# Kernel tuning notes

Measured on AMD Instinct MI355X. Metric: run time of the kernel, lower is better.

Reference implementation:

```python
import jax, jax.numpy as jnp
import numpy as np

B, N, K, C, CE, H = 2, 2048, 48, 128, 128, 128
IN = 2 * C + CE  # 384
AGG_SCALE = 30.0
LN_EPS = 1e-5


def setup_inputs() -> dict:
    key = jax.random.key(0)
    ks = jax.random.split(key, 12)
    inp = {
        "node_h": jax.random.normal(ks[0], (B, N, C), jnp.float32),
        "edge_h": jax.random.normal(ks[1], (B, N, K, CE), jnp.float32),
        "edge_index": jax.random.randint(ks[2], (B, N, K), 0, N, jnp.int64),
        # message MLP: Linear(IN,H) GELU Linear(H,H) GELU Linear(H,C)
        "W1": jax.random.normal(ks[3], (IN, H), jnp.float32) / np.sqrt(IN),
        "b1": jnp.zeros((H,), jnp.float32),
        "W2": jax.random.normal(ks[4], (H, H), jnp.float32) / np.sqrt(H),
        "b2": jnp.zeros((H,), jnp.float32),
        "W3": jax.random.normal(ks[5], (H, C), jnp.float32) / np.sqrt(H),
        "b3": jnp.zeros((C,), jnp.float32),
        "Wu": jax.random.normal(ks[6], (C, C), jnp.float32) / np.sqrt(C),
        "bu": jnp.zeros((C,), jnp.float32),
        "ln_g": jnp.ones((C,), jnp.float32),
        "ln_b": jnp.zeros((C,), jnp.float32),
    }
    return inp


def _layer_norm(x, g, b):
    mu = jnp.mean(x, axis=-1, keepdims=True)
    var = jnp.var(x, axis=-1, keepdims=True)
    return (x - mu) * jax.lax.rsqrt(var + LN_EPS) * g + b


def _gelu(x):
    return jax.nn.gelu(x, approximate=False)  # torch nn.GELU default (erf)


def reference(node_h, edge_h, edge_index, W1, b1, W2, b2, W3, b3, Wu, bu, ln_g, ln_b):
    b, n, k = edge_index.shape
    c = node_h.shape[-1]
    # gather neighbor node features: (B,N,K,C)
    node_j = jnp.take_along_axis(
        node_h, edge_index.reshape(b, n * k)[..., None], axis=1
    ).reshape(b, n, k, c)
    node_i = jnp.broadcast_to(node_h[:, :, None, :], (b, n, k, c))
    edge_packed = jnp.concatenate([node_i, node_j, edge_h], axis=-1)  # (B,N,K,IN)
    # message MLP
    h = _gelu(edge_packed @ W1 + b1)
    h = _gelu(h @ W2 + b2)
    messages = (h @ W3 + b3).sum(axis=-2) / AGG_SCALE  # (B,N,C)
    # dropout is identity in eval mode
    updated_nodes = _layer_norm(node_h + messages, ln_g, ln_b)
    node_updates = updated_nodes @ Wu + bu
    out = _layer_norm(node_h + node_updates, ln_g, ln_b)
    return out
```

## Files before the change

### kernel.cpp

```cpp
#include <hip/hip_runtime.h>
#include <hip/hip_bf16.h>
#include <math.h>

#define Bn   2
#define Nn   2048
#define Kn   48
#define Cn   128

typedef short bf16x8 __attribute__((ext_vector_type(8)));
typedef float f32x4  __attribute__((ext_vector_type(4)));

#if __has_builtin(__builtin_amdgcn_cvt_pk_bf16_f32)
#define HAS_PK 1
#endif

__device__ __forceinline__ short f2bf(float f) {
  union { float f; unsigned u; } v; v.f = f;
  unsigned r = v.u + 0x7fffu + ((v.u >> 16) & 1u);
  return (short)(r >> 16);
}

__device__ __forceinline__ unsigned pk2(float a, float b) {
#ifdef HAS_PK
  auto p = __builtin_amdgcn_cvt_pk_bf16_f32(a, b);
  return __builtin_bit_cast(unsigned, p);
#else
  return (unsigned)(unsigned short)f2bf(a) | ((unsigned)(unsigned short)f2bf(b) << 16);
#endif
}

__device__ __forceinline__ float gelu_f(float x) {
  float z = x * (-2.3021991f - 0.10294200f * x * x);
  float e = __builtin_amdgcn_exp2f(z);
  return x * __builtin_amdgcn_rcpf(1.0f + e);
}

__global__ void pack_weights(const float* __restrict__ W1,
                             const float* __restrict__ W2,
                             const float* __restrict__ W3,
                             const float* __restrict__ Wu,
                             short* __restrict__ ws) {
  int tid = blockIdx.x * blockDim.x + threadIdx.x;
  if (tid >= 192 * 64) return;
  int lane = tid & 63;
  int tile = tid >> 6;
  const float* W; short* dst;
  if (tile < 32)       { W = W1;               dst = ws; }
  else if (tile < 96)  { W = W1 + 16384;       dst = ws + 16384; tile -= 32; }
  else if (tile < 128) { W = W2;               dst = ws + 49152; tile -= 96; }
  else if (tile < 160) { W = W3;               dst = ws + 65536; tile -= 128; }
  else                 { W = Wu;               dst = ws + 81920; tile -= 160; }
  int kt = tile >> 3, nt = tile & 7;
  int n  = nt * 16 + (lane & 15);
  int k0 = kt * 32 + (lane >> 4) * 8;
  union { short s[8]; bf16x8 v; } u8;
#pragma unroll
  for (int j = 0; j < 8; j++) u8.s[j] = f2bf(W[(k0 + j) * 128 + n]);
  *reinterpret_cast<bf16x8*>(dst + (tile << 9) + lane * 8) = u8.v;
}

__device__ __forceinline__ void block_reduce2(float v1, float v2, float* red,
                                              int tid, float& o1, float& o2) {
#pragma unroll
  for (int off = 32; off >= 1; off >>= 1) {
    v1 += __shfl_xor(v1, off);
    v2 += __shfl_xor(v2, off);
  }
  if ((tid & 63) == 0) { red[tid >> 6] = v1; red[4 + (tid >> 6)] = v2; }
  __syncthreads();
  o1 = red[0] + red[1] + red[2] + red[3];
  o2 = red[4] + red[5] + red[6] + red[7];
  __syncthreads();
}

__global__ __launch_bounds__(256, 6)
void node_update_kernel(const float* __restrict__ node_h,
                        const float* __restrict__ edge_h,
                        const int*   __restrict__ edge_index,
                        const short* __restrict__ wpack,
                        const float* __restrict__ b1,
                        const float* __restrict__ b2,
                        const float* __restrict__ b3,
                        const float* __restrict__ bu,
                        const float* __restrict__ ln_g,
                        const float* __restrict__ ln_b,
                        float* __restrict__ out) {
  __shared__ __align__(16) char smem[26592];
  short* Xs    = (short*)smem;
  short* H1s   = (short*)(smem + 12288);
  short* nhb   = (short*)(smem + 24576);
  float* nhs   = (float*)(smem + 24832);
  int*   idx_s = (int*)  (smem + 25344);
  float* msg_s = (float*)(smem + 25536);
  short* hsb   = (short*)(smem + 26048);
  short* ub    = (short*)(smem + 26304);
  float* red_s = (float*)(smem + 26560);

  const int tid  = threadIdx.x;
  const int blk  = blockIdx.x;
  const int bb   = blk >> 11;
  const int lane = tid & 63;
  const int wave = tid >> 6;
  const int lr   = lane & 15;
  const int lq   = lane >> 4;

  const short* W1i = wpack;
  const short* W1e = wpack + 16384;
  const short* W2p = wpack + 49152;
  const short* W3p = wpack + 65536;
  const short* Wup = wpack + 81920;

  if (tid < 128) {
    float v = node_h[(size_t)blk * Cn + tid];
    nhs[tid] = v;
    nhb[tid] = f2bf(v);
  } else if (tid < 176) {
    idx_s[tid - 128] = edge_index[blk * Kn + (tid - 128)];
  }
  __syncthreads();

#pragma unroll
  for (int i = tid; i < 48 * 32; i += 256) {
    int r = i >> 5;
    int w = i & 31;
    const float* src = (w < 16)
        ? node_h + (size_t)(bb * Nn + idx_s[r]) * Cn + w * 8
        : edge_h + ((size_t)blk * Kn + r) * Cn + (w - 16) * 8;
    float4 v0 = *reinterpret_cast<const float4*>(src);
    float4 v1 = *reinterpret_cast<const float4*>(src + 4);
    uint4 p;
    p.x = pk2(v0.x, v0.y); p.y = pk2(v0.z, v0.w);
    p.z = pk2(v1.x, v1.y); p.w = pk2(v1.z, v1.w);
    *reinterpret_cast<uint4*>(&Xs[r * 256 + ((w ^ (r & 7)) << 3)]) = p;
  }

  f32x4 accY[2] = {};
#pragma unroll
  for (int kt = 0; kt < 4; kt++) {
    bf16x8 av = {};
    if (lr == 0) av = *reinterpret_cast<const bf16x8*>(&nhb[kt * 32 + lq * 8]);
    bf16x8 bv0 = *reinterpret_cast<const bf16x8*>(W1i + ((kt * 8 + wave * 2 + 0) << 9) + lane * 8);
    bf16x8 bv1 = *reinterpret_cast<const bf16x8*>(W1i + ((kt * 8 + wave * 2 + 1) << 9) + lane * 8);
    accY[0] = __builtin_amdgcn_mfma_f32_16x16x32_bf16(av, bv0, accY[0], 0, 0, 0);
    accY[1] = __builtin_amdgcn_mfma_f32_16x16x32_bf16(av, bv1, accY[1], 0, 0, 0);
  }
  __syncthreads();

  f32x4 acc[3][2] = {};
#pragma unroll
  for (int kt = 0; kt < 8; kt++) {
    bf16x8 bf0 = *reinterpret_cast<const bf16x8*>(W1e + ((kt * 8 + wave * 2 + 0) << 9) + lane * 8);
    bf16x8 bf1 = *reinterpret_cast<const bf16x8*>(W1e + ((kt * 8 + wave * 2 + 1) << 9) + lane * 8);
    int sw = (((kt * 4 + lq) ^ (lr & 7)) << 3);
    bf16x8 a0 = *reinterpret_cast<const bf16x8*>(&Xs[(0  + lr) * 256 + sw]);
    bf16x8 a1 = *reinterpret_cast<const bf16x8*>(&Xs[(16 + lr) * 256 + sw]);
    bf16x8 a2 = *reinterpret_cast<const bf16x8*>(&Xs[(32 + lr) * 256 + sw]);
    acc[0][0] = __builtin_amdgcn_mfma_f32_16x16x32_bf16(a0, bf0, acc[0][0], 0, 0, 0);
    acc[0][1] = __builtin_amdgcn_mfma_f32_16x16x32_bf16(a0, bf1, acc[0][1], 0, 0, 0);
    acc[1][0] = __builtin_amdgcn_mfma_f32_16x16x32_bf16(a1, bf0, acc[1][0], 0, 0, 0);
    acc[1][1] = __builtin_amdgcn_mfma_f32_16x16x32_bf16(a1, bf1, acc[1][1], 0, 0, 0);
    acc[2][0] = __builtin_amdgcn_mfma_f32_16x16x32_bf16(a2, bf0, acc[2][0], 0, 0, 0);
    acc[2][1] = __builtin_amdgcn_mfma_f32_16x16x32_bf16(a2, bf1, acc[2][1], 0, 0, 0);
  }
  __syncthreads();

#pragma unroll
  for (int j = 0; j < 2; j++) {
    int col = (wave * 2 + j) * 16 + lr;
    float yi = __shfl(accY[j][0], lr) + b1[col];
    int g = col >> 3, cl = col & 7;
#pragma unroll
    for (int mt = 0; mt < 3; mt++) {
      int r0 = mt * 16 + lq * 4;
      float g0 = gelu_f(acc[mt][j][0] + yi);
      float g1 = gelu_f(acc[mt][j][1] + yi);
      float g2 = gelu_f(acc[mt][j][2] + yi);
      float g3 = gelu_f(acc[mt][j][3] + yi);
      unsigned p01 = pk2(g0, g1), p23 = pk2(g2, g3);
      H1s[(r0 + 0) * 128 + ((g ^ ((r0 + 0) & 7)) << 3) + cl] = (short)(p01 & 0xffff);
      H1s[(r0 + 1) * 128 + ((g ^ ((r0 + 1) & 7)) << 3) + cl] = (short)(p01 >> 16);
      H1s[(r0 + 2) * 128 + ((g ^ ((r0 + 2) & 7)) << 3) + cl] = (short)(p23 & 0xffff);
      H1s[(r0 + 3) * 128 + ((g ^ ((r0 + 3) & 7)) << 3) + cl] = (short)(p23 >> 16);
    }
  }
  __syncthreads();

  f32x4 acc2[3][2] = {};
#pragma unroll
  for (int kt = 0; kt < 4; kt++) {
    bf16x8 bf0 = *reinterpret_cast<const bf16x8*>(W2p + ((kt * 8 + wave * 2 + 0) << 9) + lane * 8);
    bf16x8 bf1 = *reinterpret_cast<const bf16x8*>(W2p + ((kt * 8 + wave * 2 + 1) << 9) + lane * 8);
    int sw = (((kt * 4 + lq) ^ (lr & 7)) << 3);
    bf16x8 a0 = *reinterpret_cast<const bf16x8*>(&H1s[(0  + lr) * 128 + sw]);
    bf16x8 a1 = *reinterpret_cast<const bf16x8*>(&H1s[(16 + lr) * 128 + sw]);
    bf16x8 a2 = *reinterpret_cast<const bf16x8*>(&H1s[(32 + lr) * 128 + sw]);
    acc2[0][0] = __builtin_amdgcn_mfma_f32_16x16x32_bf16(a0, bf0, acc2[0][0], 0, 0, 0);
    acc2[0][1] = __builtin_amdgcn_mfma_f32_16x16x32_bf16(a0, bf1, acc2[0][1], 0, 0, 0);
    acc2[1][0] = __builtin_amdgcn_mfma_f32_16x16x32_bf16(a1, bf0, acc2[1][0], 0, 0, 0);
    acc2[1][1] = __builtin_amdgcn_mfma_f32_16x16x32_bf16(a1, bf1, acc2[1][1], 0, 0, 0);
    acc2[2][0] = __builtin_amdgcn_mfma_f32_16x16x32_bf16(a2, bf0, acc2[2][0], 0, 0, 0);
    acc2[2][1] = __builtin_amdgcn_mfma_f32_16x16x32_bf16(a2, bf1, acc2[2][1], 0, 0, 0);
  }
#pragma unroll
  for (int j = 0; j < 2; j++) {
    int col = (wave * 2 + j) * 16 + lr;
    float bias = b2[col];
    float s = 0.f;
#pragma unroll
    for (int mt = 0; mt < 3; mt++)
#pragma unroll
      for (int r = 0; r < 4; r++) s += gelu_f(acc2[mt][j][r] + bias);
    s += __shfl_xor(s, 16);
    s += __shfl_xor(s, 32);
    if (lq == 0) hsb[col] = f2bf(s);
  }
  __syncthreads();

  f32x4 accM[2] = {};
#pragma unroll
  for (int kt = 0; kt < 4; kt++) {
    bf16x8 av = {};
    if (lr == 0) av = *reinterpret_cast<const bf16x8*>(&hsb[kt * 32 + lq * 8]);
    bf16x8 bv0 = *reinterpret_cast<const bf16x8*>(W3p + ((kt * 8 + wave * 2 + 0) << 9) + lane * 8);
    bf16x8 bv1 = *reinterpret_cast<const bf16x8*>(W3p + ((kt * 8 + wave * 2 + 1) << 9) + lane * 8);
    accM[0] = __builtin_amdgcn_mfma_f32_16x16x32_bf16(av, bv0, accM[0], 0, 0, 0);
    accM[1] = __builtin_amdgcn_mfma_f32_16x16x32_bf16(av, bv1, accM[1], 0, 0, 0);
  }
  if (lq == 0) {
#pragma unroll
    for (int j = 0; j < 2; j++) {
      int col = (wave * 2 + j) * 16 + lr;
      msg_s[col] = (accM[j][0] + 48.0f * b3[col]) * (1.0f / 30.0f);
    }
  }
  __syncthreads();

  const int c    = tid & 127;
  const int half = tid >> 7;
  float nh = nhs[c];
  float x  = (half == 0) ? (nh + msg_s[c]) : 0.f;
  float sum, sumsq;
  block_reduce2(x, x * x, red_s, tid, sum, sumsq);
  float mu   = sum * (1.f / 128.f);
  float var  = sumsq * (1.f / 128.f) - mu * mu;
  float rstd = rsqrtf(var + 1e-5f);
  if (half == 0) ub[c] = f2bf((x - mu) * rstd * ln_g[c] + ln_b[c]);
  __syncthreads();

  f32x4 accU[2] = {};
#pragma unroll
  for (int kt = 0; kt < 4; kt++) {
    bf16x8 av = {};
    if (lr == 0) av = *reinterpret_cast<const bf16x8*>(&ub[kt * 32 + lq * 8]);
    bf16x8 bv0 = *reinterpret_cast<const bf16x8*>(Wup + ((kt * 8 + wave * 2 + 0) << 9) + lane * 8);
    bf16x8 bv1 = *reinterpret_cast<const bf16x8*>(Wup + ((kt * 8 + wave * 2 + 1) << 9) + lane * 8);
    accU[0] = __builtin_amdgcn_mfma_f32_16x16x32_bf16(av, bv0, accU[0], 0, 0, 0);
    accU[1] = __builtin_amdgcn_mfma_f32_16x16x32_bf16(av, bv1, accU[1], 0, 0, 0);
  }
  if (lq == 0) {
#pragma unroll
    for (int j = 0; j < 2; j++) {
      int col = (wave * 2 + j) * 16 + lr;
      msg_s[col] = accU[j][0] + bu[col];
    }
  }
  __syncthreads();

  float y = (half == 0) ? (nh + msg_s[c]) : 0.f;
  float sum2, sumsq2;
  block_reduce2(y, y * y, red_s, tid, sum2, sumsq2);
  float mu2   = sum2 * (1.f / 128.f);
  float var2  = sumsq2 * (1.f / 128.f) - mu2 * mu2;
  float rstd2 = rsqrtf(var2 + 1e-5f);
  if (half == 0)
    out[(size_t)blk * Cn + c] = (y - mu2) * rstd2 * ln_g[c] + ln_b[c];
}

extern "C" void kernel_launch(void* const* d_in, const int* in_sizes, int n_in,
                              void* d_out, int out_size, void* d_ws, size_t ws_size,
                              hipStream_t stream) {
  const float* node_h     = (const float*)d_in[0];
  const float* edge_h     = (const float*)d_in[1];
  const int*   edge_index = (const int*)  d_in[2];
  const float* W1 = (const float*)d_in[3];
  const float* b1 = (const float*)d_in[4];
  const float* W2 = (const float*)d_in[5];
  const float* b2 = (const float*)d_in[6];
  const float* W3 = (const float*)d_in[7];
  const float* b3 = (const float*)d_in[8];
  const float* Wu = (const float*)d_in[9];
  const float* bu = (const float*)d_in[10];
  const float* ln_g = (const float*)d_in[11];
  const float* ln_b = (const float*)d_in[12];
  float* out   = (float*)d_out;
  short* wpack = (short*)d_ws;

  pack_weights<<<48, 256, 0, stream>>>(W1, W2, W3, Wu, wpack);
  node_update_kernel<<<Bn * Nn, 256, 0, stream>>>(
      node_h, edge_h, edge_index, wpack,
      b1, b2, b3, bu, ln_g, ln_b, out);
}
```

Baseline: 215.4 us.

## Split per-node tail into batched 16-row kernel with full MFMA tiles

The per-node MLP kernel now stops after the second GELU layer and its K-sum, and writes the fp32 hidden sums into the output buffer. A new tail kernel processes 16 nodes per block. It runs W3, LayerNorm, Wu and the second LayerNorm using full 16-row MFMA tiles and per-wave shuffle reductions, instead of single-row MFMAs with block-wide reductions. This removes several barriers and wasted MFMA rows from the main kernel and cuts its LDS use. The cost is an extra launch and a global round trip of the intermediate through the output buffer.

```diff
diff --git a/kernel.cpp b/kernel.cpp
--- a/kernel.cpp
+++ b/kernel.cpp
@@ -6,6 +6,7 @@
 #define Nn   2048
 #define Kn   48
 #define Cn   128
+#define G2   16
 
 typedef short bf16x8 __attribute__((ext_vector_type(8)));
 typedef float f32x4  __attribute__((ext_vector_type(4)));
@@ -45,11 +46,11 @@
   int lane = tid & 63;
   int tile = tid >> 6;
   const float* W; short* dst;
-  if (tile < 32)       { W = W1;               dst = ws; }
-  else if (tile < 96)  { W = W1 + 16384;       dst = ws + 16384; tile -= 32; }
-  else if (tile < 128) { W = W2;               dst = ws + 49152; tile -= 96; }
-  else if (tile < 160) { W = W3;               dst = ws + 65536; tile -= 128; }
-  else                 { W = Wu;               dst = ws + 81920; tile -= 160; }
+  if (tile < 32)       { W = W1;         dst = ws; }
+  else if (tile < 96)  { W = W1 + 16384; dst = ws + 16384; tile -= 32; }
+  else if (tile < 128) { W = W2;         dst = ws + 49152; tile -= 96; }
+  else if (tile < 160) { W = W3;         dst = ws + 65536; tile -= 128; }
+  else                 { W = Wu;         dst = ws + 81920; tile -= 160; }
   int kt = tile >> 3, nt = tile & 7;
   int n  = nt * 16 + (lane & 15);
   int k0 = kt * 32 + (lane >> 4) * 8;
@@ -57,20 +58,6 @@
 #pragma unroll
   for (int j = 0; j < 8; j++) u8.s[j] = f2bf(W[(k0 + j) * 128 + n]);
   *reinterpret_cast<bf16x8*>(dst + (tile << 9) + lane * 8) = u8.v;
-}
-
-__device__ __forceinline__ void block_reduce2(float v1, float v2, float* red,
-                                              int tid, float& o1, float& o2) {
-#pragma unroll
-  for (int off = 32; off >= 1; off >>= 1) {
-    v1 += __shfl_xor(v1, off);
-    v2 += __shfl_xor(v2, off);
-  }
-  if ((tid & 63) == 0) { red[tid >> 6] = v1; red[4 + (tid >> 6)] = v2; }
-  __syncthreads();
-  o1 = red[0] + red[1] + red[2] + red[3];
-  o2 = red[4] + red[5] + red[6] + red[7];
-  __syncthreads();
 }
 
 __global__ __launch_bounds__(256, 6)
@@ -80,21 +67,12 @@
                         const short* __restrict__ wpack,
                         const float* __restrict__ b1,
                         const float* __restrict__ b2,
-                        const float* __restrict__ b3,
-                        const float* __restrict__ bu,
-                        const float* __restrict__ ln_g,
-                        const float* __restrict__ ln_b,
-                        float* __restrict__ out) {
-  __shared__ __align__(16) char smem[26592];
+                        float* __restrict__ hs_out) {
+  __shared__ __align__(16) char smem[25024];
   short* Xs    = (short*)smem;
   short* H1s   = (short*)(smem + 12288);
   short* nhb   = (short*)(smem + 24576);
-  float* nhs   = (float*)(smem + 24832);
-  int*   idx_s = (int*)  (smem + 25344);
-  float* msg_s = (float*)(smem + 25536);
-  short* hsb   = (short*)(smem + 26048);
-  short* ub    = (short*)(smem + 26304);
-  float* red_s = (float*)(smem + 26560);
+  int*   idx_s = (int*)  (smem + 24832);
 
   const int tid  = threadIdx.x;
   const int blk  = blockIdx.x;
@@ -107,31 +85,30 @@
   const short* W1i = wpack;
   const short* W1e = wpack + 16384;
   const short* W2p = wpack + 49152;
-  const short* W3p = wpack + 65536;
-  const short* Wup = wpack + 81920;
 
   if (tid < 128) {
-    float v = node_h[(size_t)blk * Cn + tid];
-    nhs[tid] = v;
-    nhb[tid] = f2bf(v);
+    nhb[tid] = f2bf(node_h[(size_t)blk * Cn + tid]);
   } else if (tid < 176) {
     idx_s[tid - 128] = edge_index[blk * Kn + (tid - 128)];
   }
   __syncthreads();
 
-#pragma unroll
-  for (int i = tid; i < 48 * 32; i += 256) {
-    int r = i >> 5;
-    int w = i & 31;
-    const float* src = (w < 16)
-        ? node_h + (size_t)(bb * Nn + idx_s[r]) * Cn + w * 8
-        : edge_h + ((size_t)blk * Kn + r) * Cn + (w - 16) * 8;
-    float4 v0 = *reinterpret_cast<const float4*>(src);
-    float4 v1 = *reinterpret_cast<const float4*>(src + 4);
-    uint4 p;
-    p.x = pk2(v0.x, v0.y); p.y = pk2(v0.z, v0.w);
-    p.z = pk2(v1.x, v1.y); p.w = pk2(v1.z, v1.w);
-    *reinterpret_cast<uint4*>(&Xs[r * 256 + ((w ^ (r & 7)) << 3)]) = p;
+  {
+    const int w  = tid & 31;
+    const int rr = tid >> 5;
+#pragma unroll
+    for (int k = 0; k < 6; k++) {
+      int r = rr + k * 8;
+      const float* src = (w < 16)
+          ? node_h + (size_t)(bb * Nn + idx_s[r]) * Cn + w * 8
+          : edge_h + ((size_t)blk * Kn + r) * Cn + (w - 16) * 8;
+      float4 v0 = *reinterpret_cast<const float4*>(src);
+      float4 v1 = *reinterpret_cast<const float4*>(src + 4);
+      uint4 p;
+      p.x = pk2(v0.x, v0.y); p.y = pk2(v0.z, v0.w);
+      p.z = pk2(v1.x, v1.y); p.w = pk2(v1.z, v1.w);
+      *reinterpret_cast<uint4*>(&Xs[r * 256 + ((w ^ (r & 7)) << 3)]) = p;
+    }
   }
 
   f32x4 accY[2] = {};
@@ -212,68 +189,135 @@
       for (int r = 0; r < 4; r++) s += gelu_f(acc2[mt][j][r] + bias);
     s += __shfl_xor(s, 16);
     s += __shfl_xor(s, 32);
-    if (lq == 0) hsb[col] = f2bf(s);
-  }
-  __syncthreads();
-
-  f32x4 accM[2] = {};
+    if (lq == 0) hs_out[(size_t)blk * Cn + col] = s;
+  }
+}
+
+__global__ __launch_bounds__(256, 4)
+void tail_kernel(const float* __restrict__ node_h,
+                 const short* __restrict__ wpack,
+                 const float* __restrict__ b3,
+                 const float* __restrict__ bu,
+                 const float* __restrict__ ln_g,
+                 const float* __restrict__ ln_b,
+                 float* __restrict__ out) {
+  __shared__ __align__(16) char sm2[24832];
+  short* hsB = (short*)sm2;
+  float* nhr = (float*)(sm2 + 4096);
+  float* xs  = (float*)(sm2 + 12288);
+  short* usB = (short*)(sm2 + 20736);
+
+  const int tid  = threadIdx.x;
+  const int lane = tid & 63;
+  const int wave = tid >> 6;
+  const int lr   = lane & 15;
+  const int lq   = lane >> 4;
+  const int n0   = blockIdx.x * G2;
+
+  const short* W3p = wpack + 65536;
+  const short* Wup = wpack + 81920;
+
+  {
+    int row = tid >> 4, seg = tid & 15;
+    const float* p = node_h + (size_t)(n0 + row) * Cn + seg * 8;
+    float4 a0 = *reinterpret_cast<const float4*>(p);
+    float4 a1 = *reinterpret_cast<const float4*>(p + 4);
+    *reinterpret_cast<float4*>(&nhr[row * 128 + seg * 8])     = a0;
+    *reinterpret_cast<float4*>(&nhr[row * 128 + seg * 8 + 4]) = a1;
+    const float* q = out + (size_t)(n0 + row) * Cn + seg * 8;
+    float4 c0 = *reinterpret_cast<const float4*>(q);
+    float4 c1 = *reinterpret_cast<const float4*>(q + 4);
+    uint4 pk;
+    pk.x = pk2(c0.x, c0.y); pk.y = pk2(c0.z, c0.w);
+    pk.z = pk2(c1.x, c1.y); pk.w = pk2(c1.z, c1.w);
+    *reinterpret_cast<uint4*>(&hsB[row * 128 + ((seg ^ (row & 7)) << 3)]) = pk;
+  }
+  __syncthreads();
+
+  f32x4 am[2] = {};
 #pragma unroll
   for (int kt = 0; kt < 4; kt++) {
-    bf16x8 av = {};
-    if (lr == 0) av = *reinterpret_cast<const bf16x8*>(&hsb[kt * 32 + lq * 8]);
+    bf16x8 av = *reinterpret_cast<const bf16x8*>(&hsB[lr * 128 + (((kt * 4 + lq) ^ (lr & 7)) << 3)]);
     bf16x8 bv0 = *reinterpret_cast<const bf16x8*>(W3p + ((kt * 8 + wave * 2 + 0) << 9) + lane * 8);
     bf16x8 bv1 = *reinterpret_cast<const bf16x8*>(W3p + ((kt * 8 + wave * 2 + 1) << 9) + lane * 8);
-    accM[0] = __builtin_amdgcn_mfma_f32_16x16x32_bf16(av, bv0, accM[0], 0, 0, 0);
-    accM[1] = __builtin_amdgcn_mfma_f32_16x16x32_bf16(av, bv1, accM[1], 0, 0, 0);
-  }
-  if (lq == 0) {
-#pragma unroll
-    for (int j = 0; j < 2; j++) {
-      int col = (wave * 2 + j) * 16 + lr;
-      msg_s[col] = (accM[j][0] + 48.0f * b3[col]) * (1.0f / 30.0f);
-    }
-  }
-  __syncthreads();
-
-  const int c    = tid & 127;
-  const int half = tid >> 7;
-  float nh = nhs[c];
-  float x  = (half == 0) ? (nh + msg_s[c]) : 0.f;
-  float sum, sumsq;
-  block_reduce2(x, x * x, red_s, tid, sum, sumsq);
-  float mu   = sum * (1.f / 128.f);
-  float var  = sumsq * (1.f / 128.f) - mu * mu;
-  float rstd = rsqrtf(var + 1e-5f);
-  if (half == 0) ub[c] = f2bf((x - mu) * rstd * ln_g[c] + ln_b[c]);
-  __syncthreads();
-
-  f32x4 accU[2] = {};
+    am[0] = __builtin_amdgcn_mfma_f32_16x16x32_bf16(av, bv0, am[0], 0, 0, 0);
+    am[1] = __builtin_amdgcn_mfma_f32_16x16x32_bf16(av, bv1, am[1], 0, 0, 0);
+  }
+#pragma unroll
+  for (int j = 0; j < 2; j++) {
+    int col = (wave * 2 + j) * 16 + lr;
+    float bb = 48.0f * b3[col];
+#pragma unroll
+    for (int r = 0; r < 4; r++) {
+      int row = lq * 4 + r;
+      xs[row * 132 + col] = nhr[row * 128 + col] + (am[j][r] + bb) * (1.0f / 30.0f);
+    }
+  }
+  __syncthreads();
+
+  const float lg1 = ln_g[lane],      lb1v = ln_b[lane];
+  const float lg2 = ln_g[lane + 64], lb2v = ln_b[lane + 64];
+#pragma unroll
+  for (int s = 0; s < 4; s++) {
+    int row = wave * 4 + s;
+    float v1 = xs[row * 132 + lane];
+    float v2 = xs[row * 132 + lane + 64];
+    float s1 = v1 + v2, s2 = v1 * v1 + v2 * v2;
+#pragma unroll
+    for (int off = 32; off >= 1; off >>= 1) {
+      s1 += __shfl_xor(s1, off);
+      s2 += __shfl_xor(s2, off);
+    }
+    float mu = s1 * (1.f / 128.f);
+    float var = s2 * (1.f / 128.f) - mu * mu;
+    float rstd = rsqrtf(var + 1e-5f);
+    unsigned u12 = pk2((v1 - mu) * rstd * lg1 + lb1v,
+                       (v2 - mu) * rstd * lg2 + lb2v);
+    int sw = (row & 7);
+    usB[row * 128 + (((lane >> 3) ^ sw) << 3) + (lane & 7)]       = (short)(u12 & 0xffff);
+    usB[row * 128 + ((((lane >> 3) + 8) ^ sw) << 3) + (lane & 7)] = (short)(u12 >> 16);
+  }
+  __syncthreads();
+
+  f32x4 au[2] = {};
 #pragma unroll
   for (int kt = 0; kt < 4; kt++) {
-    bf16x8 av = {};
-    if (lr == 0) av = *reinterpret_cast<const bf16x8*>(&ub[kt * 32 + lq * 8]);
+    bf16x8 av = *reinterpret_cast<const bf16x8*>(&usB[lr * 128 + (((kt * 4 + lq) ^ (lr & 7)) << 3)]);
     bf16x8 bv0 = *reinterpret_cast<const bf16x8*>(Wup + ((kt * 8 + wave * 2 + 0) << 9) + lane * 8);
     bf16x8 bv1 = *reinterpret_cast<const bf16x8*>(Wup + ((kt * 8 + wave * 2 + 1) << 9) + lane * 8);
-    accU[0] = __builtin_amdgcn_mfma_f32_16x16x32_bf16(av, bv0, accU[0], 0, 0, 0);
-    accU[1] = __builtin_amdgcn_mfma_f32_16x16x32_bf16(av, bv1, accU[1], 0, 0, 0);
-  }
-  if (lq == 0) {
-#pragma unroll
-    for (int j = 0; j < 2; j++) {
-      int col = (wave * 2 + j) * 16 + lr;
-      msg_s[col] = accU[j][0] + bu[col];
-    }
-  }
-  __syncthreads();
-
-  float y = (half == 0) ? (nh + msg_s[c]) : 0.f;
-  float sum2, sumsq2;
-  block_reduce2(y, y * y, red_s, tid, sum2, sumsq2);
-  float mu2   = sum2 * (1.f / 128.f);
-  float var2  = sumsq2 * (1.f / 128.f) - mu2 * mu2;
-  float rstd2 = rsqrtf(var2 + 1e-5f);
-  if (half == 0)
-    out[(size_t)blk * Cn + c] = (y - mu2) * rstd2 * ln_g[c] + ln_b[c];
+    au[0] = __builtin_amdgcn_mfma_f32_16x16x32_bf16(av, bv0, au[0], 0, 0, 0);
+    au[1] = __builtin_amdgcn_mfma_f32_16x16x32_bf16(av, bv1, au[1], 0, 0, 0);
+  }
+  __syncthreads();
+#pragma unroll
+  for (int j = 0; j < 2; j++) {
+    int col = (wave * 2 + j) * 16 + lr;
+    float bb = bu[col];
+#pragma unroll
+    for (int r = 0; r < 4; r++) {
+      int row = lq * 4 + r;
+      xs[row * 132 + col] = nhr[row * 128 + col] + au[j][r] + bb;
+    }
+  }
+  __syncthreads();
+
+#pragma unroll
+  for (int s = 0; s < 4; s++) {
+    int row = wave * 4 + s;
+    float v1 = xs[row * 132 + lane];
+    float v2 = xs[row * 132 + lane + 64];
+    float s1 = v1 + v2, s2 = v1 * v1 + v2 * v2;
+#pragma unroll
+    for (int off = 32; off >= 1; off >>= 1) {
+      s1 += __shfl_xor(s1, off);
+      s2 += __shfl_xor(s2, off);
+    }
+    float mu = s1 * (1.f / 128.f);
+    float var = s2 * (1.f / 128.f) - mu * mu;
+    float rstd = rsqrtf(var + 1e-5f);
+    out[(size_t)(n0 + row) * Cn + lane]      = (v1 - mu) * rstd * lg1 + lb1v;
+    out[(size_t)(n0 + row) * Cn + lane + 64] = (v2 - mu) * rstd * lg2 + lb2v;
+  }
 }
 
 extern "C" void kernel_launch(void* const* d_in, const int* in_sizes, int n_in,
@@ -297,6 +341,7 @@
 
   pack_weights<<<48, 256, 0, stream>>>(W1, W2, W3, Wu, wpack);
   node_update_kernel<<<Bn * Nn, 256, 0, stream>>>(
-      node_h, edge_h, edge_index, wpack,
-      b1, b2, b3, bu, ln_g, ln_b, out);
-}
+      node_h, edge_h, edge_index, wpack, b1, b2, out);
+  tail_kernel<<<(Bn * Nn) / G2, 256, 0, stream>>>(
+      node_h, wpack, b3, bu, ln_g, ln_b, out);
+}
```

New measurement: 204.6 us. 5.0% less time.
